# Kernel tuning notes

Hardware: AMD Instinct MI355X
Metric: run time of the kernel (lower is better)

## Reference

```python
import jax, jax.numpy as jnp
import numpy as np

_LOG2PI = float(np.log(2.0 * np.pi))


def setup_inputs() -> dict:
    key = jax.random.key(0)
    ks = jax.random.split(key, 9)
    B, T, S, A, O = 64, 128, 512, 16, 4096
    regime = jax.random.randint(ks[0], (B,), 0, 2).astype(jnp.float32)
    obs = jax.random.randint(ks[1], (T + 1, B), 0, O, dtype=jnp.int32)
    rewards = jax.random.normal(ks[2], (T + 1, B), jnp.float32)
    dones = jnp.zeros((T + 1, B), jnp.float32)
    actions = jax.random.randint(ks[3], (T, B), 0, A, dtype=jnp.int32)
    prior_logits = jax.random.normal(ks[4], (S,), jnp.float32)
    trans_logits = jax.random.normal(ks[5], (A, S, S), jnp.float32)
    obs_logits = jax.random.normal(ks[6], (S, O), jnp.float32)
    policy_logits = jax.random.normal(ks[7], (S, A), jnp.float32)
    r_mu = jax.random.normal(ks[8], (S,), jnp.float32)
    r_logsig = jnp.zeros((S,), jnp.float32)
    return {"regime": regime, "obs": obs, "rewards": rewards, "dones": dones,
            "actions": actions, "prior_logits": prior_logits,
            "trans_logits": trans_logits, "obs_logits": obs_logits,
            "policy_logits": policy_logits, "r_mu": r_mu, "r_logsig": r_logsig}


def _log_prob(regime, obs, rewards, dones, actions, prior_logits, trans_logits,
              obs_logits, policy_logits, r_mu, r_logsig):
    # normalized log-prob tables (tabular instantiation of AugmentedModel)
    log_prior = jax.nn.log_softmax(prior_logits)              # [S]
    log_trans = jax.nn.log_softmax(trans_logits, axis=-1)     # [A,S,S]
    log_obs = jax.nn.log_softmax(obs_logits, axis=-1)         # [S,O]
    log_pol = jax.nn.log_softmax(policy_logits, axis=-1)      # [S,A]
    lse = jax.scipy.special.logsumexp

    def emis(o, r):  # log q(o|s) + log q(r|s) -> [B,S]
        lo = log_obs.T[o]                                      # [B,S] gather
        lr = (-0.5 * (((r[:, None] - r_mu[None, :]) * jnp.exp(-r_logsig)[None, :]) ** 2)
              - r_logsig[None, :] - 0.5 * _LOG2PI)             # [B,S]
        return lo + lr

    def act_term(a, done):  # masked log q(a|s) -> [B,S]
        la = log_pol.T[a]                                      # [B,S]
        la = jnp.where((done == 1.0)[:, None], jnp.zeros_like(la), la)
        la = jnp.where((regime == 1.0)[:, None], jnp.zeros_like(la), la)
        return la

    T = actions.shape[0]
    B = regime.shape[0]

    # t = 0
    was_done = jnp.zeros((B,), rewards.dtype)
    done0 = dones[0]
    lq_sorda = log_prior[None, :] + emis(obs[0], rewards[0]) + act_term(actions[0], done0)
    lq_orda = lse(lq_sorda, axis=-1) * (1.0 - was_done)        # [B]
    log_prob = lq_orda
    lq_s_h = lq_sorda - lq_orda[:, None]
    # belief propagation through transition: [B,S,1] + [B,S,S] -> lse over prev state
    lq_snext_h = lse(lq_s_h[:, :, None] + log_trans[actions[0]], axis=1)

    def step(carry, xs):  # t = 1 .. T-1 (has an action)
        log_prob, was_done, lq_s_hprev = carry
        o, r, d, a = xs
        done = jnp.maximum(was_done, d)
        lq = lq_s_hprev + emis(o, r) + act_term(a, done)
        lq_orda = lse(lq, axis=-1) * (1.0 - was_done)
        log_prob = jnp.where(jnp.isinf(log_prob), log_prob, log_prob + lq_orda)
        lq_s_h = lq - lq_orda[:, None]
        lq_snext = lse(lq_s_h[:, :, None] + log_trans[a], axis=1)
        return (log_prob, done, lq_snext), None

    xs = (obs[1:T], rewards[1:T], dones[1:T], actions[1:T])
    (log_prob, was_done, lq_s_hprev), _ = jax.lax.scan(
        step, (log_prob, done0, lq_snext_h), xs)

    # final step t = T (no action term)
    lq = lq_s_hprev + emis(obs[T], rewards[T])
    lq_ord = lse(lq, axis=-1) * (1.0 - was_done)
    log_prob = jnp.where(jnp.isinf(log_prob), log_prob, log_prob + lq_ord)
    return log_prob


def reference(regime, obs, rewards, dones, actions, prior_logits, trans_logits,
              obs_logits, policy_logits, r_mu, r_logsig):
    return _log_prob(regime, obs, rewards, dones, actions, prior_logits,
                     trans_logits, obs_logits, policy_logits, r_mu, r_logsig)
```

## Files before the change

### kernel.cpp

```cpp
#include <hip/hip_runtime.h>
#include <math.h>

#define DI __device__ __forceinline__

constexpr int BB = 64;
constexpr int TT = 128;
constexpr int SS = 512;
constexpr int AA = 16;
constexpr int OO = 4096;
constexpr float LOG2PI = 1.8378770664093453f;
constexpr float LOG4096 = 8.317766166719343f;

typedef float f32x4 __attribute__((ext_vector_type(4)));

DI void lds_barrier() {
    asm volatile("s_waitcnt lgkmcnt(0)\n\ts_barrier" ::: "memory");
}

DI unsigned int f32_to_e4m3(float x) {
    unsigned int u = __float_as_uint(x);
    unsigned int lsb = (u >> 20) & 1u;
    unsigned int rounded = u + 0x7ffffu + lsb;
    int e8 = (int)(rounded >> 23) - 120;
    unsigned int m3 = (rounded >> 20) & 7u;
    unsigned int norm = ((unsigned int)e8 << 3) | m3;
    int sub = __float2int_rn(x * 512.0f);
    return (e8 <= 0) ? (unsigned int)sub : norm;
}

DI float bflyMax(float v) {
#pragma unroll
    for (int off = 32; off; off >>= 1) v = fmaxf(v, __shfl_xor(v, off));
    return v;
}
DI float bflySum(float v) {
#pragma unroll
    for (int off = 32; off; off >>= 1) v += __shfl_xor(v, off);
    return v;
}
DI float halfMax(float v) {
#pragma unroll
    for (int off = 16; off; off >>= 1) v = fmaxf(v, __shfl_xor(v, off));
    return v;
}
DI float halfSum(float v) {
#pragma unroll
    for (int off = 16; off; off >>= 1) v += __shfl_xor(v, off);
    return v;
}

__global__ __launch_bounds__(1024) void k_pre(const float* __restrict__ tl,
                                              unsigned char* __restrict__ PB,
                                              const float* __restrict__ ol,
                                              float* __restrict__ mo,
                                              float* __restrict__ lo) {
    __shared__ unsigned char lds[16384];
    __shared__ float wr2[16], ws2[16];
    const int bid = blockIdx.x;
    const int tid = threadIdx.x;

    if (bid < 256) {
        const int a = bid >> 4;
        const int kt = bid & 15;
        const int r = tid >> 5;
        const int nt = tid & 31;
        const int k = kt * 32 + r;
        const float* row = tl + ((size_t)a * SS + k) * SS + nt * 16;

        float x[16];
#pragma unroll
        for (int i = 0; i < 4; ++i) {
            float4 v = ((const float4*)row)[i];
            x[4 * i] = v.x; x[4 * i + 1] = v.y; x[4 * i + 2] = v.z; x[4 * i + 3] = v.w;
        }
        float mx = -INFINITY;
#pragma unroll
        for (int i = 0; i < 16; ++i) mx = fmaxf(mx, x[i]);
        mx = halfMax(mx);
        float e[16];
        float sm = 0.f;
#pragma unroll
        for (int i = 0; i < 16; ++i) { e[i] = __expf(x[i] - mx); sm += e[i]; }
        sm = halfSum(sm);
        const float scale = 256.0f / sm;

        const int base = (nt >> 1) * 1024 + ((r >> 3) * 16) * 16 + (nt & 1) * 8 + (r & 7);
#pragma unroll
        for (int i = 0; i < 16; ++i) {
            lds[base + i * 16] = (unsigned char)f32_to_e4m3(e[i] * scale);
        }
        __syncthreads();

        ulonglong2* dst = (ulonglong2*)(PB + (size_t)(a * 16 + kt) * 16384);
        dst[tid] = ((const ulonglong2*)lds)[tid];
    } else {
        const int r = tid >> 8;
        const int u = tid & 255;
        const int wir = (tid >> 6) & 3;
        const int srow = (bid - 256) * 4 + r;
        const float* in = ol + (size_t)srow * OO;

        float mx = -INFINITY;
#pragma unroll
        for (int k = 0; k < 16; ++k) mx = fmaxf(mx, in[u + k * 256]);
        mx = bflyMax(mx);
        if ((tid & 63) == 0) wr2[r * 4 + wir] = mx;
        __syncthreads();
        float m = fmaxf(fmaxf(wr2[r * 4], wr2[r * 4 + 1]),
                        fmaxf(wr2[r * 4 + 2], wr2[r * 4 + 3]));
        float sm = 0.f;
#pragma unroll
        for (int k = 0; k < 16; ++k) sm += __expf(in[u + k * 256] - m);
        sm = bflySum(sm);
        if ((tid & 63) == 0) ws2[r * 4 + wir] = sm;
        __syncthreads();
        if (u == 0) {
            float sum = ws2[r * 4] + ws2[r * 4 + 1] + ws2[r * 4 + 2] + ws2[r * 4 + 3];
            mo[srow] = m;
            lo[srow] = __logf(sum);
        }
    }
}

__global__ __launch_bounds__(256) void k_obsT(const float* __restrict__ ol,
                                              const float* __restrict__ mo,
                                              const float* __restrict__ lo,
                                              float* __restrict__ obsT) {
    __shared__ float tile[64][65];
    const int tO = blockIdx.x % (OO / 64);
    const int tS = blockIdx.x / (OO / 64);
    const int o0 = tO * 64, s0 = tS * 64;
    const int cc = threadIdx.x & 63, rr = threadIdx.x >> 6;
#pragma unroll
    for (int j = 0; j < 16; ++j) {
        int r = rr + j * 4;
        tile[r][cc] = ol[(size_t)(s0 + r) * OO + o0 + cc] - mo[s0 + r] - lo[s0 + r];
    }
    __syncthreads();
#pragma unroll
    for (int j = 0; j < 16; ++j) {
        int r = rr + j * 4;
        obsT[(size_t)(o0 + r) * SS + s0 + cc] = tile[cc][r];
    }
}

__global__ __launch_bounds__(512, 2) void k_main(
    const float* __restrict__ regime, const int* __restrict__ obs,
    const float* __restrict__ rewards, const float* __restrict__ dones,
    const int* __restrict__ actions, const float* __restrict__ prior_logits,
    const unsigned char* __restrict__ PB, const float* __restrict__ obsT,
    const float* __restrict__ policy_logits, const float* __restrict__ r_mu,
    const float* __restrict__ r_logsig, float* __restrict__ out) {
    __shared__ float wrm[8], wrs[8];
    __shared__ unsigned char p8[4 * 144 + 16];
    __shared__ int obs_l[TT + 1];
    __shared__ float rew_l[TT + 1];
    __shared__ float done_l[TT + 1];
    __shared__ int act_l[TT];

    const int b = blockIdx.x;
    const int tid = threadIdx.x;
    const int wv = tid >> 6, lane = tid & 63, quad = lane >> 4;
    const int s = tid;
    const int wvl16 = wv * 2048 + lane * 16;
    const int p8idx = ((s >> 3) & 3) * 144 + (s >> 5) * 8 + (s & 7);

    if (tid <= TT) {
        obs_l[tid] = obs[tid * BB + b];
        rew_l[tid] = rewards[tid * BB + b];
        done_l[tid] = dones[tid * BB + b];
        if (tid < TT) act_l[tid] = actions[tid * BB + b];
    }
    float la16[16];
    {
        const float4* pr4 = (const float4*)(policy_logits + (size_t)s * AA);
        float4 v0 = pr4[0], v1 = pr4[1], v2 = pr4[2], v3 = pr4[3];
        la16[0] = v0.x; la16[1] = v0.y; la16[2] = v0.z; la16[3] = v0.w;
        la16[4] = v1.x; la16[5] = v1.y; la16[6] = v1.z; la16[7] = v1.w;
        la16[8] = v2.x; la16[9] = v2.y; la16[10] = v2.z; la16[11] = v2.w;
        la16[12] = v3.x; la16[13] = v3.y; la16[14] = v3.z; la16[15] = v3.w;
        float mx = la16[0];
#pragma unroll
        for (int i = 1; i < 16; ++i) mx = fmaxf(mx, la16[i]);
        float sm = 0.f;
#pragma unroll
        for (int i = 0; i < 16; ++i) sm += __expf(la16[i] - mx);
        float ls = mx + __logf(sm);
#pragma unroll
        for (int i = 0; i < 16; ++i) la16[i] -= ls;
    }
    const float rm = r_mu[s];
    const float rls = r_logsig[s];
    const float inv_sig = __expf(-rls);
    const float reg = regime[b];

    float px = prior_logits[s];
    {
        float wm0 = bflyMax(px);
        if (lane == 0) wrm[wv] = wm0;
    }
    lds_barrier();
    float pm = wrm[0];
#pragma unroll
    for (int i = 1; i < 8; ++i) pm = fmaxf(pm, wrm[i]);
    {
        float ws0 = bflySum(__expf(px - pm));
        if (lane == 0) wrs[wv] = ws0;
    }
    lds_barrier();
    float psum = wrs[0];
#pragma unroll
    for (int i = 1; i < 8; ++i) psum += wrs[i];
    float base_reg = px - pm - __logf(psum);

    ulonglong2 fA[8], fB[8], gA[8], gB[8];
    {
        const int a0 = __builtin_amdgcn_readfirstlane(act_l[0]);
        const unsigned char* P0 = PB + (size_t)a0 * (16 * 16384) + wvl16;
#pragma unroll
        for (int c = 0; c < 8; ++c) {
            fA[c] = *(const ulonglong2*)(P0 + c * 16384);
            fB[c] = *(const ulonglong2*)(P0 + c * 16384 + 1024);
        }
    }
    float obsv = obsT[(size_t)obs_l[0] * SS + s];

    float log_prob = 0.f;
    float was_done = 0.f;

#define CHUNK_L(c, CA, CB)                                                      \
    {                                                                           \
        long af = *(const long long*)(p8 + quad * 144 + (c) * 8);               \
        acc0 = __builtin_amdgcn_mfma_f32_16x16x32_fp8_fp8((long)CA[(c)].x, af, acc0, 0, 0, 0); \
        acc1 = __builtin_amdgcn_mfma_f32_16x16x32_fp8_fp8((long)CA[(c)].y, af, acc1, 0, 0, 0); \
        acc2 = __builtin_amdgcn_mfma_f32_16x16x32_fp8_fp8((long)CB[(c)].x, af, acc2, 0, 0, 0); \
        acc3 = __builtin_amdgcn_mfma_f32_16x16x32_fp8_fp8((long)CB[(c)].y, af, acc3, 0, 0, 0); \
        CA[(c)] = *(const ulonglong2*)(Pw_ + ((c) + 8) * 16384);                \
        CB[(c)] = *(const ulonglong2*)(Pw_ + ((c) + 8) * 16384 + 1024);         \
    }
#define CHUNK_H(c, CA, CB, NA, NB)                                              \
    {                                                                           \
        long af = *(const long long*)(p8 + quad * 144 + (c) * 8);               \
        acc0 = __builtin_amdgcn_mfma_f32_16x16x32_fp8_fp8((long)CA[(c) - 8].x, af, acc0, 0, 0, 0); \
        acc1 = __builtin_amdgcn_mfma_f32_16x16x32_fp8_fp8((long)CA[(c) - 8].y, af, acc1, 0, 0, 0); \
        acc2 = __builtin_amdgcn_mfma_f32_16x16x32_fp8_fp8((long)CB[(c) - 8].x, af, acc2, 0, 0, 0); \
        acc3 = __builtin_amdgcn_mfma_f32_16x16x32_fp8_fp8((long)CB[(c) - 8].y, af, acc3, 0, 0, 0); \
        NA[(c) - 8] = *(const ulonglong2*)(Pn_ + ((c) - 8) * 16384);            \
        NB[(c) - 8] = *(const ulonglong2*)(Pn_ + ((c) - 8) * 16384 + 1024);     \
    }

#define STEP(T, CA, CB, NA, NB)                                                 \
    {                                                                           \
        const int t_ = (T);                                                     \
        const float r_ = rew_l[t_];                                             \
        const int a_ = __builtin_amdgcn_readfirstlane(act_l[t_]);               \
        const float d_ = done_l[t_];                                            \
        const float done_ = fmaxf(was_done, d_);                                \
        const unsigned char* Pw_ = PB + (size_t)a_ * (16 * 16384) + wvl16;      \
        const int tn_ = (t_ + 1 < TT) ? t_ + 1 : 0;                             \
        const int an_ = __builtin_amdgcn_readfirstlane(act_l[tn_]);             \
        const unsigned char* Pn_ = PB + (size_t)an_ * (16 * 16384) + wvl16;     \
        float obsv_next_ = obsT[(size_t)obs_l[t_ + 1] * SS + s];                \
                \
        float diff_ = (r_ - rm) * inv_sig;                                      \
        float emis_ = obsv - 0.5f * diff_ * diff_ - rls - 0.5f * LOG2PI;        \
        float la_ = la16[0];                                                    \
        _Pragma("unroll")                                                       \
        for (int i = 1; i < 16; ++i) la_ = (a_ == i) ? la16[i] : la_;           \
        if (done_ == 1.0f || reg == 1.0f) la_ = 0.f;                            \
        float lq_ = base_reg + emis_ + la_;                                     \
        float wmax_ = bflyMax(lq_);                                             \
        if (lane == 0) wrm[wv] = wmax_;                                         \
        lds_barrier();                                                  \
        float m_ = wrm[0];                                                      \
        _Pragma("unroll")                                                       \
        for (int i = 1; i < 8; ++i) m_ = fmaxf(m_, wrm[i]);                     \
        float exv_ = __expf(lq_ - m_);                                          \
        p8[p8idx] = (unsigned char)f32_to_e4m3(exv_ * 16.0f);                   \
        float wsum_ = bflySum(exv_);                                            \
        if (lane == 0) wrs[wv] = wsum_;                                         \
        lds_barrier();                                   \
        float sum_ = wrs[0];                                                    \
        _Pragma("unroll")                                                       \
        for (int i = 1; i < 8; ++i) sum_ += wrs[i];                             \
        float lse_ = m_ + __logf(sum_);                                         \
        float lqo_ = lse_ * (1.0f - was_done);                                  \
        if (!isinf(log_prob)) log_prob += lqo_;                                 \
        was_done = done_;                                                       \
        \
        const float basev_ = m_ - lqo_ - LOG4096;                               \
        f32x4 acc0 = {0.f, 0.f, 0.f, 0.f};                                      \
        f32x4 acc1 = {0.f, 0.f, 0.f, 0.f};                                      \
        f32x4 acc2 = {0.f, 0.f, 0.f, 0.f};                                      \
        f32x4 acc3 = {0.f, 0.f, 0.f, 0.f};                                      \
        CHUNK_L(0, CA, CB)  CHUNK_L(1, CA, CB)  CHUNK_L(2, CA, CB)              \
        CHUNK_L(3, CA, CB)  CHUNK_L(4, CA, CB)  CHUNK_L(5, CA, CB)              \
        CHUNK_L(6, CA, CB)  CHUNK_L(7, CA, CB)                                  \
        CHUNK_H(8, CA, CB, NA, NB)   CHUNK_H(9, CA, CB, NA, NB)                 \
        CHUNK_H(10, CA, CB, NA, NB)  CHUNK_H(11, CA, CB, NA, NB)                \
        CHUNK_H(12, CA, CB, NA, NB)  CHUNK_H(13, CA, CB, NA, NB)                \
        CHUNK_H(14, CA, CB, NA, NB)  CHUNK_H(15, CA, CB, NA, NB)                \
           \
        float t0_ = __shfl(acc0[0], lane & 15);                                 \
        float t1_ = __shfl(acc1[0], lane & 15);                                 \
        float t2_ = __shfl(acc2[0], lane & 15);                                 \
        float t3_ = __shfl(acc3[0], lane & 15);                                 \
        float av_ = quad == 0 ? t0_ : (quad == 1 ? t1_ : (quad == 2 ? t2_ : t3_)); \
        base_reg = basev_ + __logf(av_);                                        \
        obsv = obsv_next_;                                                      \
        asm volatile("" ::: "memory");      \
    }

    for (int t = 0; t < TT; t += 2) {
        STEP(t, fA, fB, gA, gB)
        STEP(t + 1, gA, gB, fA, fB)
    }
#undef STEP
#undef CHUNK_L
#undef CHUNK_H

    {
        const float r = rew_l[TT];
        float diff = (r - rm) * inv_sig;
        float emis = obsv - 0.5f * diff * diff - rls - 0.5f * LOG2PI;
        float lq = base_reg + emis;
        float wmax = bflyMax(lq);
        if (lane == 0) wrm[wv] = wmax;
        lds_barrier();
        float m = wrm[0];
#pragma unroll
        for (int i = 1; i < 8; ++i) m = fmaxf(m, wrm[i]);
        float wsum = bflySum(__expf(lq - m));
        if (lane == 0) wrs[wv] = wsum;
        lds_barrier();
        float sum = wrs[0];
#pragma unroll
        for (int i = 1; i < 8; ++i) sum += wrs[i];
        float lse = m + __logf(sum);
        float lq_ord = lse * (1.0f - was_done);
        if (!isinf(log_prob)) log_prob += lq_ord;
    }

    if (tid == 0) out[b] = log_prob;
}

extern "C" void kernel_launch(void* const* d_in, const int* in_sizes, int n_in,
                              void* d_out, int out_size, void* d_ws, size_t ws_size,
                              hipStream_t stream) {
    const float* regime = (const float*)d_in[0];
    const int* obs = (const int*)d_in[1];
    const float* rewards = (const float*)d_in[2];
    const float* dones = (const float*)d_in[3];
    const int* actions = (const int*)d_in[4];
    const float* prior_logits = (const float*)d_in[5];
    const float* trans_logits = (const float*)d_in[6];
    const float* obs_logits = (const float*)d_in[7];
    const float* policy_logits = (const float*)d_in[8];
    const float* r_mu = (const float*)d_in[9];
    const float* r_logsig = (const float*)d_in[10];
    float* out = (float*)d_out;

    char* ws = (char*)d_ws;
    unsigned char* PB = (unsigned char*)ws;
    float* obsT = (float*)(ws + (size_t)AA * SS * SS);
    float* mo = (float*)(ws + (size_t)AA * SS * SS + (size_t)OO * SS * 4);
    float* lo = mo + SS;

    k_pre<<<384, 1024, 0, stream>>>(trans_logits, PB, obs_logits, mo, lo);
    k_obsT<<<(OO / 64) * (SS / 64), 256, 0, stream>>>(obs_logits, mo, lo, obsT);
    k_main<<<BB, 512, 0, stream>>>(regime, obs, rewards, dones, actions, prior_logits,
                                   PB, obsT, policy_logits, r_mu, r_logsig, out);
}
```

Before: 466.5 us.

## Fuse obs log-softmax normalization and transpose into preprocessing kernel

Drops the separate k_obsT launch and the mo/lo intermediates. Each preprocessing block now owns 16 state rows: one wavefront per row computes the logsumexp, then the block writes the normalized, transposed obsT directly with float4 stores of 16 consecutive states per observation. This saves one kernel launch and the intermediate round trip, but the obs blocks drop from 128 to 32, which cuts parallelism in that part of the work.

```diff
diff --git a/kernel.cpp b/kernel.cpp
--- a/kernel.cpp
+++ b/kernel.cpp
@@ -52,10 +52,9 @@
 __global__ __launch_bounds__(1024) void k_pre(const float* __restrict__ tl,
                                               unsigned char* __restrict__ PB,
                                               const float* __restrict__ ol,
-                                              float* __restrict__ mo,
-                                              float* __restrict__ lo) {
+                                              float* __restrict__ obsT) {
     __shared__ unsigned char lds[16384];
-    __shared__ float wr2[16], ws2[16];
+    __shared__ float mls[16];
     const int bid = blockIdx.x;
     const int tid = threadIdx.x;
 
@@ -94,53 +93,38 @@
         ulonglong2* dst = (ulonglong2*)(PB + (size_t)(a * 16 + kt) * 16384);
         dst[tid] = ((const ulonglong2*)lds)[tid];
     } else {
-        const int r = tid >> 8;
-        const int u = tid & 255;
-        const int wir = (tid >> 6) & 3;
-        const int srow = (bid - 256) * 4 + r;
-        const float* in = ol + (size_t)srow * OO;
+        const int s0 = (bid - 256) * 16;
+        const int rw = tid >> 6;
+        const int lane = tid & 63;
+        const float* in = ol + (size_t)(s0 + rw) * OO;
 
         float mx = -INFINITY;
-#pragma unroll
-        for (int k = 0; k < 16; ++k) mx = fmaxf(mx, in[u + k * 256]);
+#pragma unroll 4
+        for (int k = 0; k < 64; ++k) mx = fmaxf(mx, in[lane + k * 64]);
         mx = bflyMax(mx);
-        if ((tid & 63) == 0) wr2[r * 4 + wir] = mx;
+        float sm = 0.f;
+#pragma unroll 4
+        for (int k = 0; k < 64; ++k) sm += __expf(in[lane + k * 64] - mx);
+        sm = bflySum(sm);
+        if (lane == 0) mls[rw] = mx + __logf(sm);
         __syncthreads();
-        float m = fmaxf(fmaxf(wr2[r * 4], wr2[r * 4 + 1]),
-                        fmaxf(wr2[r * 4 + 2], wr2[r * 4 + 3]));
-        float sm = 0.f;
-#pragma unroll
-        for (int k = 0; k < 16; ++k) sm += __expf(in[u + k * 256] - m);
-        sm = bflySum(sm);
-        if ((tid & 63) == 0) ws2[r * 4 + wir] = sm;
-        __syncthreads();
-        if (u == 0) {
-            float sum = ws2[r * 4] + ws2[r * 4 + 1] + ws2[r * 4 + 2] + ws2[r * 4 + 3];
-            mo[srow] = m;
-            lo[srow] = __logf(sum);
+
+        float ml[16];
+#pragma unroll
+        for (int j = 0; j < 16; ++j) ml[j] = mls[j];
+#pragma unroll
+        for (int oo = 0; oo < 4; ++oo) {
+            const int o = tid + oo * 1024;
+            float w[16];
+#pragma unroll
+            for (int j = 0; j < 16; ++j)
+                w[j] = ol[(size_t)(s0 + j) * OO + o] - ml[j];
+            float4* dst = (float4*)(obsT + (size_t)o * SS + s0);
+            dst[0] = make_float4(w[0], w[1], w[2], w[3]);
+            dst[1] = make_float4(w[4], w[5], w[6], w[7]);
+            dst[2] = make_float4(w[8], w[9], w[10], w[11]);
+            dst[3] = make_float4(w[12], w[13], w[14], w[15]);
         }
-    }
-}
-
-__global__ __launch_bounds__(256) void k_obsT(const float* __restrict__ ol,
-                                              const float* __restrict__ mo,
-                                              const float* __restrict__ lo,
-                                              float* __restrict__ obsT) {
-    __shared__ float tile[64][65];
-    const int tO = blockIdx.x % (OO / 64);
-    const int tS = blockIdx.x / (OO / 64);
-    const int o0 = tO * 64, s0 = tS * 64;
-    const int cc = threadIdx.x & 63, rr = threadIdx.x >> 6;
-#pragma unroll
-    for (int j = 0; j < 16; ++j) {
-        int r = rr + j * 4;
-        tile[r][cc] = ol[(size_t)(s0 + r) * OO + o0 + cc] - mo[s0 + r] - lo[s0 + r];
-    }
-    __syncthreads();
-#pragma unroll
-    for (int j = 0; j < 16; ++j) {
-        int r = rr + j * 4;
-        obsT[(size_t)(o0 + r) * SS + s0 + cc] = tile[cc][r];
     }
 }
 
@@ -363,11 +347,8 @@
     char* ws = (char*)d_ws;
     unsigned char* PB = (unsigned char*)ws;
     float* obsT = (float*)(ws + (size_t)AA * SS * SS);
-    float* mo = (float*)(ws + (size_t)AA * SS * SS + (size_t)OO * SS * 4);
-    float* lo = mo + SS;
-
-    k_pre<<<384, 1024, 0, stream>>>(trans_logits, PB, obs_logits, mo, lo);
-    k_obsT<<<(OO / 64) * (SS / 64), 256, 0, stream>>>(obs_logits, mo, lo, obsT);
+
+    k_pre<<<288, 1024, 0, stream>>>(trans_logits, PB, obs_logits, obsT);
     k_main<<<BB, 512, 0, stream>>>(regime, obs, rewards, dones, actions, prior_logits,
                                    PB, obsT, policy_logits, r_mu, r_logsig, out);
 }
```

Measured after the change: 486.9 us. +4.4%, slower.
